# Kernel tuning notes

Measured on AMD Instinct MI355X. Metric: run time of the kernel, lower is better.

Reference implementation:

```python
import jax, jax.numpy as jnp
import numpy as np

INPUT_DIM = 1024
OUTPUT_DIM = 512


def setup_inputs() -> dict:
    key = jax.random.key(0)
    ks = jax.random.split(key, 7)
    s_in = 1.0 / np.sqrt(INPUT_DIM)
    x = jax.random.normal(ks[0], (8, 2048, INPUT_DIM), dtype=jnp.float32)
    Wq = jax.random.uniform(ks[1], (INPUT_DIM, INPUT_DIM), jnp.float32, -s_in, s_in)
    bq = jax.random.uniform(ks[2], (INPUT_DIM,), jnp.float32, -s_in, s_in)
    Wk = jax.random.uniform(ks[3], (INPUT_DIM, INPUT_DIM), jnp.float32, -s_in, s_in)
    bk = jax.random.uniform(ks[4], (INPUT_DIM,), jnp.float32, -s_in, s_in)
    Wv = jax.random.uniform(ks[5], (INPUT_DIM, OUTPUT_DIM), jnp.float32, -s_in, s_in)
    bv = jax.random.uniform(ks[6], (OUTPUT_DIM,), jnp.float32, -s_in, s_in)
    return {"x": x, "Wq": Wq, "bq": bq, "Wk": Wk, "bk": bk, "Wv": Wv, "bv": bv}


def reference(x, Wq, bq, Wk, bk, Wv, bv):
    # x: [B, S, D]
    B, S, D = x.shape
    scale = 1.0 / jnp.sqrt(jnp.asarray(D, x.dtype))
    Q = jnp.einsum('bsd,de->bse', x, Wq) + bq  # [B,S,D]
    K = jnp.einsum('bsd,de->bse', x, Wk) + bk  # [B,S,D]
    V = jnp.einsum('bsd,de->bse', x, Wv) + bv  # [B,S,O]
    scores = jnp.einsum('bqd,bkd->bqk', Q, K) * scale  # [B,S,S]
    causal = jnp.tril(jnp.ones((S, S), dtype=bool))
    scores = jnp.where(causal, scores, -jnp.inf)
    attn = jax.nn.softmax(scores, axis=-1)
    return jnp.einsum('bqk,bko->bqo', attn, V)  # [B,S,O]
```

## Files before the change

### kernel.cpp

```cpp
#include <hip/hip_runtime.h>
#include <hip/hip_bf16.h>
#include <stdint.h>
#include <cmath>

typedef __bf16 bf16x8 __attribute__((ext_vector_type(8)));
typedef float f32x4 __attribute__((ext_vector_type(4)));

#define NB 8
#define NS 2048
#define ND 1024
#define NO 512

__device__ __forceinline__ unsigned short f2bf(float f) {
  union { float f; uint32_t u; } c;
  c.f = f;
  uint32_t u = c.u;
  uint32_t r = (u + 0x7fffu + ((u >> 16) & 1u)) >> 16;
  return (unsigned short)r;
}

__device__ __forceinline__ void glds16(const void* g, void* l) {
  __builtin_amdgcn_global_load_lds(
      (const __attribute__((address_space(1))) unsigned int*)g,
      (__attribute__((address_space(3))) unsigned int*)l, 16, 0, 0);
}

__global__ void cast_x_kernel(const float* __restrict__ in,
                              unsigned short* __restrict__ out, int n8) {
  int i = blockIdx.x * blockDim.x + threadIdx.x;
  if (i >= n8) return;
  const float4* p = reinterpret_cast<const float4*>(in) + 2 * (size_t)i;
  float4 a = p[0], b = p[1];
  union { unsigned short us[8]; int4 v; } r;
  r.us[0] = f2bf(a.x); r.us[1] = f2bf(a.y); r.us[2] = f2bf(a.z); r.us[3] = f2bf(a.w);
  r.us[4] = f2bf(b.x); r.us[5] = f2bf(b.y); r.us[6] = f2bf(b.z); r.us[7] = f2bf(b.w);
  reinterpret_cast<int4*>(out)[i] = r.v;
}

__global__ void transpose_cast_kernel(const float* __restrict__ in,
                                      unsigned short* __restrict__ out,
                                      int R, int C) {
  __shared__ unsigned short t[32][33];
  int bx = blockIdx.x;
  int by = blockIdx.y;
  int x = threadIdx.x & 31, y = threadIdx.x >> 5;
#pragma unroll
  for (int j = 0; j < 4; j++) {
    int r = by * 32 + y + j * 8;
    int c = bx * 32 + x;
    t[y + j * 8][x] = f2bf(in[(size_t)r * C + c]);
  }
  __syncthreads();
#pragma unroll
  for (int j = 0; j < 4; j++) {
    int c = bx * 32 + y + j * 8;
    int r = by * 32 + x;
    out[(size_t)c * R + r] = t[x][y + j * 8];
  }
}

__global__ void transpose_v_kernel(const unsigned short* __restrict__ in,
                                   unsigned short* __restrict__ out) {
  __shared__ unsigned short t[32][33];
  int b = blockIdx.z;
  int bo = blockIdx.x;
  int bs = blockIdx.y;
  const unsigned short* ib = in + (size_t)b * NS * NO;
  unsigned short* ob = out + (size_t)b * NO * NS;
  int x = threadIdx.x & 31, y = threadIdx.x >> 5;
#pragma unroll
  for (int j = 0; j < 4; j++)
    t[y + j * 8][x] = ib[(size_t)(bs * 32 + y + j * 8) * NO + bo * 32 + x];
  __syncthreads();
#pragma unroll
  for (int j = 0; j < 4; j++)
    ob[(size_t)(bo * 32 + y + j * 8) * NS + bs * 32 + x] = t[x][y + j * 8];
}

__global__ __launch_bounds__(256, 2) void gemm_bias_kernel(
    const unsigned short* __restrict__ A, const unsigned short* __restrict__ Bt,
    const float* __restrict__ bias, unsigned short* __restrict__ C,
    int M, int N, int K) {
  __shared__ unsigned short lA[2][128 * 32];
  __shared__ unsigned short lB[2][128 * 32];
  const int tid = threadIdx.x;
  const int w = tid >> 6, l = tid & 63;
  const int m0 = blockIdx.x * 128, n0 = blockIdx.y * 128;
  const int wr = w >> 1, wc = w & 1;
  const int lr16 = l & 15, lg = l >> 4;
  f32x4 acc[4][4];
#pragma unroll
  for (int i = 0; i < 4; i++)
#pragma unroll
    for (int j = 0; j < 4; j++) acc[i][j] = (f32x4){0.f, 0.f, 0.f, 0.f};
  const int srow = w * 32 + (l >> 2);
  const int sk = (l & 3) * 8;
  auto stage = [&](int buf, int k0) {
#pragma unroll
    for (int j = 0; j < 2; j++) {
      glds16(&A[(size_t)(m0 + srow + j * 16) * K + k0 + sk], &lA[buf][w * 1024 + j * 512]);
      glds16(&Bt[(size_t)(n0 + srow + j * 16) * K + k0 + sk], &lB[buf][w * 1024 + j * 512]);
    }
  };
  const int nt = K >> 5;
  stage(0, 0);
  __syncthreads();
  int cur = 0;
  for (int t = 0; t < nt; ++t) {
    if (t + 1 < nt) stage(cur ^ 1, (t + 1) * 32);
    bf16x8 af[4], bfr[4];
#pragma unroll
    for (int mi = 0; mi < 4; mi++)
      af[mi] = *reinterpret_cast<const bf16x8*>(&lA[cur][(wr * 64 + mi * 16 + lr16) * 32 + lg * 8]);
#pragma unroll
    for (int ni = 0; ni < 4; ni++)
      bfr[ni] = *reinterpret_cast<const bf16x8*>(&lB[cur][(wc * 64 + ni * 16 + lr16) * 32 + lg * 8]);
#pragma unroll
    for (int mi = 0; mi < 4; mi++)
#pragma unroll
      for (int ni = 0; ni < 4; ni++)
        acc[mi][ni] = __builtin_amdgcn_mfma_f32_16x16x32_bf16(af[mi], bfr[ni], acc[mi][ni], 0, 0, 0);
    __syncthreads();
    cur ^= 1;
  }
#pragma unroll
  for (int ni = 0; ni < 4; ni++) {
    int col = n0 + wc * 64 + ni * 16 + lr16;
    float bv = bias[col];
#pragma unroll
    for (int mi = 0; mi < 4; mi++) {
#pragma unroll
      for (int i = 0; i < 4; i++) {
        int row = m0 + wr * 64 + mi * 16 + lg * 4 + i;
        C[(size_t)row * N + col] = f2bf(acc[mi][ni][i] + bv);
      }
    }
  }
}

__global__ __launch_bounds__(256, 1) void flash_split_kernel(
    const unsigned short* __restrict__ Q, const unsigned short* __restrict__ K,
    const unsigned short* __restrict__ Vt, unsigned short* __restrict__ opart,
    float* __restrict__ ml) {
  __shared__ unsigned short ubuf[4 * 8192];
  __shared__ unsigned short lP[64 * 64];
  const int bid = blockIdx.x;
  const int b = bid & 7;
  const int t = bid >> 3;
  int qi, half;
  if (t < 32) { qi = 31 - (t >> 1); half = t & 1; }
  else        { int u2 = t - 32; qi = u2 >> 1; half = u2 & 1; }
  const int nkt = qi + 1;
  const int h = (qi + 2) >> 1;
  const int lo = half ? h : 0;
  const int hi = half ? nkt : h;
  const int total = 12 * (hi - lo);

  const int tid = threadIdx.x, w = tid >> 6, l = tid & 63;
  const unsigned short* Qb = Q + (size_t)b * NS * ND;
  const unsigned short* Kb = K + (size_t)b * NS * ND;
  const unsigned short* Vb = Vt + (size_t)b * NO * NS;
  const int q0 = qi * 64;
  const int lr16 = l & 15, lg = l >> 4;

  bf16x8 qreg[32];
  {
    const unsigned short* qrow = &Qb[(size_t)(q0 + w * 16 + lr16) * ND + lg * 8];
#pragma unroll
    for (int c = 0; c < 32; c++)
      qreg[c] = *reinterpret_cast<const bf16x8*>(qrow + c * 32);
  }

  f32x4 acc_o[32];
#pragma unroll
  for (int f = 0; f < 32; f++) acc_o[f] = (f32x4){0.f, 0.f, 0.f, 0.f};
  float m_s[4], l_s[4];
#pragma unroll
  for (int i = 0; i < 4; i++) { m_s[i] = -INFINITY; l_s[i] = 0.f; }
  const float sc = 0.03125f * 1.4426950408889634f;

  auto stage = [&](int g) {
    int ki = lo + g / 12, u = g - (g / 12) * 12;
    int k0 = ki * 64;
    unsigned short* dst = &ubuf[(g & 3) * 8192];
    if (u < 8) {
#pragma unroll
      for (int j = 0; j < 4; j++) {
        int row = j * 16 + w * 4 + (l >> 4);
        int gl = (l & 15) ^ (row & 7);
        glds16(&Kb[(size_t)(k0 + row) * ND + u * 128 + gl * 8],
               dst + j * 2048 + w * 512);
      }
    } else {
      int nc = u - 8;
#pragma unroll
      for (int j = 0; j < 4; j++) {
        int row = j * 32 + w * 8 + (l >> 3);
        int gl = (l & 7) ^ (row & 7);
        glds16(&Vb[(size_t)(nc * 128 + row) * NS + k0 + gl * 8],
               dst + j * 2048 + w * 512);
      }
    }
  };

  if (total > 0) {
    stage(0);
    if (total > 1) stage(1);
    if (total > 2) stage(2);

    bf16x8 pa0 = {}, pa1 = {};
    for (int ki = lo; ki < hi; ++ki) {
      const int gbase = (ki - lo) * 12;
      f32x4 accs[4];
#pragma unroll
      for (int f = 0; f < 4; f++) accs[f] = (f32x4){0.f, 0.f, 0.f, 0.f};

#pragma unroll
      for (int u = 0; u < 12; ++u) {
        const int g = gbase + u;
        const int rem = total - g;
        if (rem > 2)
          asm volatile("s_waitcnt vmcnt(8) lgkmcnt(0)\ns_barrier" ::: "memory");
        else if (rem > 1)
          asm volatile("s_waitcnt vmcnt(4) lgkmcnt(0)\ns_barrier" ::: "memory");
        else
          asm volatile("s_waitcnt vmcnt(0) lgkmcnt(0)\ns_barrier" ::: "memory");
        if (g + 3 < total) stage(g + 3);
        const unsigned short* bp = &ubuf[(g & 3) * 8192];

        if (u < 8) {
#pragma unroll
          for (int ks = 0; ks < 4; ks++) {
            bf16x8 a = qreg[u * 4 + ks];
#pragma unroll
            for (int fn = 0; fn < 4; fn++) {
              int row = fn * 16 + lr16;
              int p = (ks * 4 + lg) ^ (row & 7);
              bf16x8 bb = *reinterpret_cast<const bf16x8*>(&bp[row * 128 + p * 8]);
              accs[fn] = __builtin_amdgcn_mfma_f32_16x16x32_bf16(a, bb, accs[fn], 0, 0, 0);
            }
          }
          if (u == 7) {
            const bool diag = (ki == qi);
            float alpha[4];
#pragma unroll
            for (int i = 0; i < 4; i++) {
              float v0 = accs[0][i] * sc, v1 = accs[1][i] * sc;
              float v2 = accs[2][i] * sc, v3 = accs[3][i] * sc;
              if (diag) {
                int qr = w * 16 + lg * 4 + i;
                if (lr16 > qr) v0 = -INFINITY;
                if (16 + lr16 > qr) v1 = -INFINITY;
                if (32 + lr16 > qr) v2 = -INFINITY;
                if (48 + lr16 > qr) v3 = -INFINITY;
              }
              float pm = fmaxf(fmaxf(v0, v1), fmaxf(v2, v3));
              pm = fmaxf(pm, __shfl_xor(pm, 1));
              pm = fmaxf(pm, __shfl_xor(pm, 2));
              pm = fmaxf(pm, __shfl_xor(pm, 4));
              pm = fmaxf(pm, __shfl_xor(pm, 8));
              float mn = fmaxf(m_s[i], pm);
              float al = exp2f(m_s[i] - mn);
              float p0 = exp2f(v0 - mn), p1 = exp2f(v1 - mn);
              float p2 = exp2f(v2 - mn), p3 = exp2f(v3 - mn);
              float rs = (p0 + p1) + (p2 + p3);
              rs += __shfl_xor(rs, 1);
              rs += __shfl_xor(rs, 2);
              rs += __shfl_xor(rs, 4);
              rs += __shfl_xor(rs, 8);
              l_s[i] = l_s[i] * al + rs;
              m_s[i] = mn;
              alpha[i] = al;
              accs[0][i] = p0; accs[1][i] = p1; accs[2][i] = p2; accs[3][i] = p3;
            }
#pragma unroll
            for (int f = 0; f < 32; f++)
#pragma unroll
              for (int i = 0; i < 4; i++) acc_o[f][i] *= alpha[i];
#pragma unroll
            for (int fn = 0; fn < 4; fn++)
#pragma unroll
              for (int i = 0; i < 4; i++) {
                int pr = w * 16 + lg * 4 + i;
                int pg = (fn * 2 + (lr16 >> 3)) ^ (pr & 7);
                lP[pr * 64 + pg * 8 + (lr16 & 7)] = f2bf(accs[fn][i]);
              }
          }
        } else {
          const int nc = u - 8;
          if (u == 8) {
            int prow = w * 16 + lr16;
            pa0 = *reinterpret_cast<const bf16x8*>(&lP[prow * 64 + ((0 + lg) ^ (prow & 7)) * 8]);
            pa1 = *reinterpret_cast<const bf16x8*>(&lP[prow * 64 + ((4 + lg) ^ (prow & 7)) * 8]);
          }
#pragma unroll
          for (int fc = 0; fc < 8; fc++) {
            int row = fc * 16 + lr16;
            int p0i = (0 + lg) ^ (row & 7);
            int p1i = (4 + lg) ^ (row & 7);
            bf16x8 b0 = *reinterpret_cast<const bf16x8*>(&bp[row * 64 + p0i * 8]);
            bf16x8 b1 = *reinterpret_cast<const bf16x8*>(&bp[row * 64 + p1i * 8]);
            int f = nc * 8 + fc;
            acc_o[f] = __builtin_amdgcn_mfma_f32_16x16x32_bf16(pa0, b0, acc_o[f], 0, 0, 0);
            acc_o[f] = __builtin_amdgcn_mfma_f32_16x16x32_bf16(pa1, b1, acc_o[f], 0, 0, 0);
          }
        }
      }
    }
  }

  const int slot = (qi * 2 + half) * 8 + b;
  unsigned short* op = opart + (size_t)slot * 64 * 512;
#pragma unroll
  for (int nc = 0; nc < 4; nc++)
#pragma unroll
    for (int fc = 0; fc < 8; fc++)
#pragma unroll
      for (int i = 0; i < 4; i++) {
        int row = w * 16 + lg * 4 + i;
        int col = nc * 128 + fc * 16 + lr16;
        op[(size_t)row * 512 + col] = f2bf(acc_o[nc * 8 + fc][i]);
      }
  float* mlp = ml + slot * 128;
  if (lr16 == 0) {
#pragma unroll
    for (int i = 0; i < 4; i++) {
      int row = w * 16 + lg * 4 + i;
      mlp[row] = m_s[i];
      mlp[64 + row] = l_s[i];
    }
  }
}

__global__ __launch_bounds__(256) void combine_kernel(
    const unsigned short* __restrict__ opart, const float* __restrict__ ml,
    float* __restrict__ Out) {
  const int bid = blockIdx.x;
  const int b = bid & 7, qi = bid >> 3;
  const int tid = threadIdx.x;
  const int c8 = (tid & 63) * 8;
  const int rbase = (tid >> 6) * 16;
  const int sA = (qi * 2 + 0) * 8 + b;
  const int sB = sA + 8;
  const unsigned short* OA = opart + (size_t)sA * 32768;
  const unsigned short* OB = opart + (size_t)sB * 32768;
  const float* mlA = ml + sA * 128;
  const float* mlB = ml + sB * 128;
  float* ob = Out + ((size_t)b * NS + qi * 64) * NO;
#pragma unroll
  for (int rr = 0; rr < 16; rr++) {
    int r = rbase + rr;
    float mA = mlA[r], lA = mlA[64 + r];
    float mB = mlB[r], lB = mlB[64 + r];
    float m = fmaxf(mA, mB);
    float eA = exp2f(mA - m);
    float eB = (mB == -INFINITY) ? 0.f : exp2f(mB - m);
    float inv = 1.0f / (eA * lA + eB * lB);
    bf16x8 a = *reinterpret_cast<const bf16x8*>(&OA[(size_t)r * 512 + c8]);
    bf16x8 bb = *reinterpret_cast<const bf16x8*>(&OB[(size_t)r * 512 + c8]);
    float4 o0, o1;
    o0.x = ((float)a[0] * eA + (float)bb[0] * eB) * inv;
    o0.y = ((float)a[1] * eA + (float)bb[1] * eB) * inv;
    o0.z = ((float)a[2] * eA + (float)bb[2] * eB) * inv;
    o0.w = ((float)a[3] * eA + (float)bb[3] * eB) * inv;
    o1.x = ((float)a[4] * eA + (float)bb[4] * eB) * inv;
    o1.y = ((float)a[5] * eA + (float)bb[5] * eB) * inv;
    o1.z = ((float)a[6] * eA + (float)bb[6] * eB) * inv;
    o1.w = ((float)a[7] * eA + (float)bb[7] * eB) * inv;
    float4* dst = reinterpret_cast<float4*>(&ob[(size_t)r * 512 + c8]);
    dst[0] = o0;
    dst[1] = o1;
  }
}

extern "C" void kernel_launch(void* const* d_in, const int* in_sizes, int n_in,
                              void* d_out, int out_size, void* d_ws, size_t ws_size,
                              hipStream_t stream) {
  const float* x = (const float*)d_in[0];
  const float* Wq = (const float*)d_in[1];
  const float* bq = (const float*)d_in[2];
  const float* Wk = (const float*)d_in[3];
  const float* bk = (const float*)d_in[4];
  const float* Wv = (const float*)d_in[5];
  const float* bv = (const float*)d_in[6];
  float* out = (float*)d_out;
  char* ws = (char*)d_ws;

  unsigned short* xb  = (unsigned short*)(ws + 0);
  unsigned short* wqt = (unsigned short*)(ws + 33554432);
  unsigned short* wkt = (unsigned short*)(ws + 35651584);
  unsigned short* wvt = (unsigned short*)(ws + 37748736);
  unsigned short* Qb  = (unsigned short*)(ws + 38797312);
  unsigned short* Kb  = (unsigned short*)(ws + 72351744);
  unsigned short* Vb  = (unsigned short*)(ws + 105906176);
  unsigned short* Vtb = (unsigned short*)(ws + 122683392);
  unsigned short* opart = xb;
  float* mlbuf = (float*)(ws + 105906176);

  cast_x_kernel<<<8192, 256, 0, stream>>>(x, xb, (NB * NS * ND) / 8);
  transpose_cast_kernel<<<dim3(32, 32), 256, 0, stream>>>(Wq, wqt, ND, ND);
  transpose_cast_kernel<<<dim3(32, 32), 256, 0, stream>>>(Wk, wkt, ND, ND);
  transpose_cast_kernel<<<dim3(16, 32), 256, 0, stream>>>(Wv, wvt, ND, NO);
  gemm_bias_kernel<<<dim3(128, 8), 256, 0, stream>>>(xb, wqt, bq, Qb, NB * NS, ND, ND);
  gemm_bias_kernel<<<dim3(128, 8), 256, 0, stream>>>(xb, wkt, bk, Kb, NB * NS, ND, ND);
  gemm_bias_kernel<<<dim3(128, 4), 256, 0, stream>>>(xb, wvt, bv, Vb, NB * NS, NO, ND);
  transpose_v_kernel<<<dim3(16, 64, 8), 256, 0, stream>>>(Vb, Vtb);
  flash_split_kernel<<<512, 256, 0, stream>>>(Qb, Kb, Vtb, opart, mlbuf);
  combine_kernel<<<256, 256, 0, stream>>>(opart, mlbuf, out);
}
```

Measured before the change: 487.8 us.

## Use 128-row query tiles with 512-thread blocks in split flash attention

Flash kernel moves from 64-row query tiles with 4 waves to 128-row tiles with 8 waves. K/V tiles staged in shared memory are now shared across twice as many query rows, halving global K/V traffic per query. Each block's KV range is split evenly in half, and the causal mask is applied per wave based on absolute positions. The combine kernel is resized to match. The change also halves the number of blocks, 256 of them at 512 threads, which may hurt load balance and occupancy. Register pressure under launch_bounds(512,2) is a risk.

Result: slower. 655.1 us (+34.3%).

```diff
diff --git a/kernel.cpp b/kernel.cpp
--- a/kernel.cpp
+++ b/kernel.cpp
@@ -138,29 +138,27 @@
   }
 }
 
-__global__ __launch_bounds__(256, 1) void flash_split_kernel(
+__global__ __launch_bounds__(512, 2) void flash_split_kernel(
     const unsigned short* __restrict__ Q, const unsigned short* __restrict__ K,
     const unsigned short* __restrict__ Vt, unsigned short* __restrict__ opart,
     float* __restrict__ ml) {
   __shared__ unsigned short ubuf[4 * 8192];
-  __shared__ unsigned short lP[64 * 64];
+  __shared__ unsigned short lP[128 * 64];
   const int bid = blockIdx.x;
   const int b = bid & 7;
   const int t = bid >> 3;
-  int qi, half;
-  if (t < 32) { qi = 31 - (t >> 1); half = t & 1; }
-  else        { int u2 = t - 32; qi = u2 >> 1; half = u2 & 1; }
-  const int nkt = qi + 1;
-  const int h = (qi + 2) >> 1;
-  const int lo = half ? h : 0;
-  const int hi = half ? nkt : h;
+  const int qj = t >> 1;
+  const int half = t & 1;
+  const int ntk = (qj + 1) * 2;
+  const int lo = half ? (qj + 1) : 0;
+  const int hi = half ? ntk : (qj + 1);
   const int total = 12 * (hi - lo);
 
   const int tid = threadIdx.x, w = tid >> 6, l = tid & 63;
   const unsigned short* Qb = Q + (size_t)b * NS * ND;
   const unsigned short* Kb = K + (size_t)b * NS * ND;
   const unsigned short* Vb = Vt + (size_t)b * NO * NS;
-  const int q0 = qi * 64;
+  const int q0 = qj * 128;
   const int lr16 = l & 15, lg = l >> 4;
 
   bf16x8 qreg[32];
@@ -176,7 +174,7 @@
   for (int f = 0; f < 32; f++) acc_o[f] = (f32x4){0.f, 0.f, 0.f, 0.f};
   float m_s[4], l_s[4];
 #pragma unroll
-  for (int i = 0; i < 4; i++) { m_s[i] = -INFINITY; l_s[i] = 0.f; }
+  for (int i = 0; i < 4; i++) { m_s[i] = -1.0e30f; l_s[i] = 0.f; }
   const float sc = 0.03125f * 1.4426950408889634f;
 
   auto stage = [&](int g) {
@@ -185,132 +183,131 @@
     unsigned short* dst = &ubuf[(g & 3) * 8192];
     if (u < 8) {
 #pragma unroll
-      for (int j = 0; j < 4; j++) {
-        int row = j * 16 + w * 4 + (l >> 4);
+      for (int ps = 0; ps < 2; ps++) {
+        int row = ps * 32 + w * 4 + (l >> 4);
         int gl = (l & 15) ^ (row & 7);
         glds16(&Kb[(size_t)(k0 + row) * ND + u * 128 + gl * 8],
-               dst + j * 2048 + w * 512);
+               dst + ps * 4096 + w * 512);
       }
     } else {
       int nc = u - 8;
 #pragma unroll
-      for (int j = 0; j < 4; j++) {
-        int row = j * 32 + w * 8 + (l >> 3);
+      for (int ps = 0; ps < 2; ps++) {
+        int row = ps * 64 + w * 8 + (l >> 3);
         int gl = (l & 7) ^ (row & 7);
         glds16(&Vb[(size_t)(nc * 128 + row) * NS + k0 + gl * 8],
-               dst + j * 2048 + w * 512);
+               dst + ps * 4096 + w * 512);
       }
     }
   };
 
-  if (total > 0) {
-    stage(0);
-    if (total > 1) stage(1);
-    if (total > 2) stage(2);
-
-    bf16x8 pa0 = {}, pa1 = {};
-    for (int ki = lo; ki < hi; ++ki) {
-      const int gbase = (ki - lo) * 12;
-      f32x4 accs[4];
-#pragma unroll
-      for (int f = 0; f < 4; f++) accs[f] = (f32x4){0.f, 0.f, 0.f, 0.f};
-
-#pragma unroll
-      for (int u = 0; u < 12; ++u) {
-        const int g = gbase + u;
-        const int rem = total - g;
-        if (rem > 2)
-          asm volatile("s_waitcnt vmcnt(8) lgkmcnt(0)\ns_barrier" ::: "memory");
-        else if (rem > 1)
-          asm volatile("s_waitcnt vmcnt(4) lgkmcnt(0)\ns_barrier" ::: "memory");
-        else
-          asm volatile("s_waitcnt vmcnt(0) lgkmcnt(0)\ns_barrier" ::: "memory");
-        if (g + 3 < total) stage(g + 3);
-        const unsigned short* bp = &ubuf[(g & 3) * 8192];
-
-        if (u < 8) {
-#pragma unroll
-          for (int ks = 0; ks < 4; ks++) {
-            bf16x8 a = qreg[u * 4 + ks];
-#pragma unroll
-            for (int fn = 0; fn < 4; fn++) {
-              int row = fn * 16 + lr16;
-              int p = (ks * 4 + lg) ^ (row & 7);
-              bf16x8 bb = *reinterpret_cast<const bf16x8*>(&bp[row * 128 + p * 8]);
-              accs[fn] = __builtin_amdgcn_mfma_f32_16x16x32_bf16(a, bb, accs[fn], 0, 0, 0);
+  stage(0);
+  stage(1);
+  if (total > 2) stage(2);
+
+  bf16x8 pa0 = {}, pa1 = {};
+  for (int ki = lo; ki < hi; ++ki) {
+    const int k0 = ki * 64;
+    const int gbase = (ki - lo) * 12;
+    f32x4 accs[4];
+#pragma unroll
+    for (int f = 0; f < 4; f++) accs[f] = (f32x4){0.f, 0.f, 0.f, 0.f};
+
+#pragma unroll
+    for (int u = 0; u < 12; ++u) {
+      const int g = gbase + u;
+      const int rem = total - g;
+      if (rem > 2)
+        asm volatile("s_waitcnt vmcnt(4) lgkmcnt(0)\ns_barrier" ::: "memory");
+      else if (rem > 1)
+        asm volatile("s_waitcnt vmcnt(2) lgkmcnt(0)\ns_barrier" ::: "memory");
+      else
+        asm volatile("s_waitcnt vmcnt(0) lgkmcnt(0)\ns_barrier" ::: "memory");
+      if (g + 3 < total) stage(g + 3);
+      const unsigned short* bp = &ubuf[(g & 3) * 8192];
+
+      if (u < 8) {
+#pragma unroll
+        for (int ks = 0; ks < 4; ks++) {
+          bf16x8 a = qreg[u * 4 + ks];
+#pragma unroll
+          for (int fn = 0; fn < 4; fn++) {
+            int row = fn * 16 + lr16;
+            int p = (ks * 4 + lg) ^ (row & 7);
+            bf16x8 bb = *reinterpret_cast<const bf16x8*>(&bp[row * 128 + p * 8]);
+            accs[fn] = __builtin_amdgcn_mfma_f32_16x16x32_bf16(a, bb, accs[fn], 0, 0, 0);
+          }
+        }
+        if (u == 7) {
+          const bool needMask = (k0 + 63 > q0 + w * 16);
+          float alpha[4];
+#pragma unroll
+          for (int i = 0; i < 4; i++) {
+            float v0 = accs[0][i] * sc, v1 = accs[1][i] * sc;
+            float v2 = accs[2][i] * sc, v3 = accs[3][i] * sc;
+            if (needMask) {
+              int qr = q0 + w * 16 + lg * 4 + i - k0;
+              if (lr16 > qr) v0 = -INFINITY;
+              if (16 + lr16 > qr) v1 = -INFINITY;
+              if (32 + lr16 > qr) v2 = -INFINITY;
+              if (48 + lr16 > qr) v3 = -INFINITY;
             }
+            float pm = fmaxf(fmaxf(v0, v1), fmaxf(v2, v3));
+            pm = fmaxf(pm, __shfl_xor(pm, 1));
+            pm = fmaxf(pm, __shfl_xor(pm, 2));
+            pm = fmaxf(pm, __shfl_xor(pm, 4));
+            pm = fmaxf(pm, __shfl_xor(pm, 8));
+            float mn = fmaxf(m_s[i], pm);
+            float al = exp2f(m_s[i] - mn);
+            float p0 = exp2f(v0 - mn), p1 = exp2f(v1 - mn);
+            float p2 = exp2f(v2 - mn), p3 = exp2f(v3 - mn);
+            float rs = (p0 + p1) + (p2 + p3);
+            rs += __shfl_xor(rs, 1);
+            rs += __shfl_xor(rs, 2);
+            rs += __shfl_xor(rs, 4);
+            rs += __shfl_xor(rs, 8);
+            l_s[i] = l_s[i] * al + rs;
+            m_s[i] = mn;
+            alpha[i] = al;
+            accs[0][i] = p0; accs[1][i] = p1; accs[2][i] = p2; accs[3][i] = p3;
           }
-          if (u == 7) {
-            const bool diag = (ki == qi);
-            float alpha[4];
+#pragma unroll
+          for (int f = 0; f < 32; f++)
+#pragma unroll
+            for (int i = 0; i < 4; i++) acc_o[f][i] *= alpha[i];
+#pragma unroll
+          for (int fn = 0; fn < 4; fn++)
 #pragma unroll
             for (int i = 0; i < 4; i++) {
-              float v0 = accs[0][i] * sc, v1 = accs[1][i] * sc;
-              float v2 = accs[2][i] * sc, v3 = accs[3][i] * sc;
-              if (diag) {
-                int qr = w * 16 + lg * 4 + i;
-                if (lr16 > qr) v0 = -INFINITY;
-                if (16 + lr16 > qr) v1 = -INFINITY;
-                if (32 + lr16 > qr) v2 = -INFINITY;
-                if (48 + lr16 > qr) v3 = -INFINITY;
-              }
-              float pm = fmaxf(fmaxf(v0, v1), fmaxf(v2, v3));
-              pm = fmaxf(pm, __shfl_xor(pm, 1));
-              pm = fmaxf(pm, __shfl_xor(pm, 2));
-              pm = fmaxf(pm, __shfl_xor(pm, 4));
-              pm = fmaxf(pm, __shfl_xor(pm, 8));
-              float mn = fmaxf(m_s[i], pm);
-              float al = exp2f(m_s[i] - mn);
-              float p0 = exp2f(v0 - mn), p1 = exp2f(v1 - mn);
-              float p2 = exp2f(v2 - mn), p3 = exp2f(v3 - mn);
-              float rs = (p0 + p1) + (p2 + p3);
-              rs += __shfl_xor(rs, 1);
-              rs += __shfl_xor(rs, 2);
-              rs += __shfl_xor(rs, 4);
-              rs += __shfl_xor(rs, 8);
-              l_s[i] = l_s[i] * al + rs;
-              m_s[i] = mn;
-              alpha[i] = al;
-              accs[0][i] = p0; accs[1][i] = p1; accs[2][i] = p2; accs[3][i] = p3;
+              int pr = w * 16 + lg * 4 + i;
+              int pg = (fn * 2 + (lr16 >> 3)) ^ (pr & 7);
+              lP[pr * 64 + pg * 8 + (lr16 & 7)] = f2bf(accs[fn][i]);
             }
-#pragma unroll
-            for (int f = 0; f < 32; f++)
-#pragma unroll
-              for (int i = 0; i < 4; i++) acc_o[f][i] *= alpha[i];
-#pragma unroll
-            for (int fn = 0; fn < 4; fn++)
-#pragma unroll
-              for (int i = 0; i < 4; i++) {
-                int pr = w * 16 + lg * 4 + i;
-                int pg = (fn * 2 + (lr16 >> 3)) ^ (pr & 7);
-                lP[pr * 64 + pg * 8 + (lr16 & 7)] = f2bf(accs[fn][i]);
-              }
-          }
-        } else {
-          const int nc = u - 8;
-          if (u == 8) {
-            int prow = w * 16 + lr16;
-            pa0 = *reinterpret_cast<const bf16x8*>(&lP[prow * 64 + ((0 + lg) ^ (prow & 7)) * 8]);
-            pa1 = *reinterpret_cast<const bf16x8*>(&lP[prow * 64 + ((4 + lg) ^ (prow & 7)) * 8]);
-          }
-#pragma unroll
-          for (int fc = 0; fc < 8; fc++) {
-            int row = fc * 16 + lr16;
-            int p0i = (0 + lg) ^ (row & 7);
-            int p1i = (4 + lg) ^ (row & 7);
-            bf16x8 b0 = *reinterpret_cast<const bf16x8*>(&bp[row * 64 + p0i * 8]);
-            bf16x8 b1 = *reinterpret_cast<const bf16x8*>(&bp[row * 64 + p1i * 8]);
-            int f = nc * 8 + fc;
-            acc_o[f] = __builtin_amdgcn_mfma_f32_16x16x32_bf16(pa0, b0, acc_o[f], 0, 0, 0);
-            acc_o[f] = __builtin_amdgcn_mfma_f32_16x16x32_bf16(pa1, b1, acc_o[f], 0, 0, 0);
-          }
+        }
+      } else {
+        const int nc = u - 8;
+        if (u == 8) {
+          int prow = w * 16 + lr16;
+          pa0 = *reinterpret_cast<const bf16x8*>(&lP[prow * 64 + ((0 + lg) ^ (prow & 7)) * 8]);
+          pa1 = *reinterpret_cast<const bf16x8*>(&lP[prow * 64 + ((4 + lg) ^ (prow & 7)) * 8]);
+        }
+#pragma unroll
+        for (int fc = 0; fc < 8; fc++) {
+          int row = fc * 16 + lr16;
+          int p0i = (0 + lg) ^ (row & 7);
+          int p1i = (4 + lg) ^ (row & 7);
+          bf16x8 b0 = *reinterpret_cast<const bf16x8*>(&bp[row * 64 + p0i * 8]);
+          bf16x8 b1 = *reinterpret_cast<const bf16x8*>(&bp[row * 64 + p1i * 8]);
+          int f = nc * 8 + fc;
+          acc_o[f] = __builtin_amdgcn_mfma_f32_16x16x32_bf16(pa0, b0, acc_o[f], 0, 0, 0);
+          acc_o[f] = __builtin_amdgcn_mfma_f32_16x16x32_bf16(pa1, b1, acc_o[f], 0, 0, 0);
         }
       }
     }
   }
 
-  const int slot = (qi * 2 + half) * 8 + b;
-  unsigned short* op = opart + (size_t)slot * 64 * 512;
+  const int slot = (qj * 2 + half) * 8 + b;
+  unsigned short* op = opart + (size_t)slot * 128 * 512;
 #pragma unroll
   for (int nc = 0; nc < 4; nc++)
 #pragma unroll
@@ -321,13 +318,13 @@
         int col = nc * 128 + fc * 16 + lr16;
         op[(size_t)row * 512 + col] = f2bf(acc_o[nc * 8 + fc][i]);
       }
-  float* mlp = ml + slot * 128;
+  float* mlp = ml + slot * 256;
   if (lr16 == 0) {
 #pragma unroll
     for (int i = 0; i < 4; i++) {
       int row = w * 16 + lg * 4 + i;
       mlp[row] = m_s[i];
-      mlp[64 + row] = l_s[i];
+      mlp[128 + row] = l_s[i];
     }
   }
 }
@@ -336,25 +333,25 @@
     const unsigned short* __restrict__ opart, const float* __restrict__ ml,
     float* __restrict__ Out) {
   const int bid = blockIdx.x;
-  const int b = bid & 7, qi = bid >> 3;
+  const int b = bid & 7, qj = bid >> 3;
   const int tid = threadIdx.x;
   const int c8 = (tid & 63) * 8;
-  const int rbase = (tid >> 6) * 16;
-  const int sA = (qi * 2 + 0) * 8 + b;
+  const int rbase = (tid >> 6) * 32;
+  const int sA = (qj * 2 + 0) * 8 + b;
   const int sB = sA + 8;
-  const unsigned short* OA = opart + (size_t)sA * 32768;
-  const unsigned short* OB = opart + (size_t)sB * 32768;
-  const float* mlA = ml + sA * 128;
-  const float* mlB = ml + sB * 128;
-  float* ob = Out + ((size_t)b * NS + qi * 64) * NO;
-#pragma unroll
-  for (int rr = 0; rr < 16; rr++) {
+  const unsigned short* OA = opart + (size_t)sA * 65536;
+  const unsigned short* OB = opart + (size_t)sB * 65536;
+  const float* mlA = ml + sA * 256;
+  const float* mlB = ml + sB * 256;
+  float* ob = Out + ((size_t)b * NS + qj * 128) * NO;
+#pragma unroll
+  for (int rr = 0; rr < 32; rr++) {
     int r = rbase + rr;
-    float mA = mlA[r], lA = mlA[64 + r];
-    float mB = mlB[r], lB = mlB[64 + r];
+    float mA = mlA[r], lA = mlA[128 + r];
+    float mB = mlB[r], lB = mlB[128 + r];
     float m = fmaxf(mA, mB);
     float eA = exp2f(mA - m);
-    float eB = (mB == -INFINITY) ? 0.f : exp2f(mB - m);
+    float eB = exp2f(mB - m);
     float inv = 1.0f / (eA * lA + eB * lB);
     bf16x8 a = *reinterpret_cast<const bf16x8*>(&OA[(size_t)r * 512 + c8]);
     bf16x8 bb = *reinterpret_cast<const bf16x8*>(&OB[(size_t)r * 512 + c8]);
@@ -405,6 +402,6 @@
   gemm_bias_kernel<<<dim3(128, 8), 256, 0, stream>>>(xb, wkt, bk, Kb, NB * NS, ND, ND);
   gemm_bias_kernel<<<dim3(128, 4), 256, 0, stream>>>(xb, wvt, bv, Vb, NB * NS, NO, ND);
   transpose_v_kernel<<<dim3(16, 64, 8), 256, 0, stream>>>(Vb, Vtb);
-  flash_split_kernel<<<512, 256, 0, stream>>>(Qb, Kb, Vtb, opart, mlbuf);
-  combine_kernel<<<256, 256, 0, stream>>>(opart, mlbuf, out);
-}
+  flash_split_kernel<<<256, 512, 0, stream>>>(Qb, Kb, Vtb, opart, mlbuf);
+  combine_kernel<<<128, 256, 0, stream>>>(opart, mlbuf, out);
+}
```
